# Performance work log

Measured on AMD Instinct MI355X. Metric: run time of the kernel, lower is better.

## Reference

```python
import jax, jax.numpy as jnp
import numpy as np

D = 128      # embedding_dim
E = 50000    # positive edges per metapath
S = 16       # negative samples per edge
N_A = 100000 # nodes of type A (head type of both metapaths)
N_B = 50000  # nodes of type B (tail type of metapath 1)


def setup_inputs() -> dict:
    key = jax.random.key(0)
    ks = jax.random.split(key, 10)
    emb_A = jax.random.normal(ks[0], (N_A, D), dtype=jnp.float32)
    emb_B = jax.random.normal(ks[1], (N_B, D), dtype=jnp.float32)
    # nn.init.uniform_(a=-1, b=1)
    rel_emb = jax.random.uniform(ks[2], (2, D, D), dtype=jnp.float32, minval=-1.0, maxval=1.0)
    edge_index_m0 = jax.random.randint(ks[3], (2, E), 0, N_A)  # A -> A
    edge_index_m1 = jnp.stack([
        jax.random.randint(ks[4], (E,), 0, N_A),               # heads: type A
        jax.random.randint(ks[5], (E,), 0, N_B),               # tails: type B
    ])
    neg_head_m0 = jax.random.randint(ks[6], (E, S), 0, N_A)
    neg_head_m1 = jax.random.randint(ks[7], (E, S), 0, N_A)
    neg_tail_m0 = jax.random.randint(ks[8], (E, S), 0, N_A)
    neg_tail_m1 = jax.random.randint(ks[9], (E, S), 0, N_B)
    return dict(emb_A=emb_A, emb_B=emb_B, rel_emb=rel_emb,
                edge_index_m0=edge_index_m0, edge_index_m1=edge_index_m1,
                neg_head_m0=neg_head_m0, neg_head_m1=neg_head_m1,
                neg_tail_m0=neg_tail_m0, neg_tail_m1=neg_tail_m1)


# The torch module computes score = (A K B^T).sum(dim=1); summing the [E,E]
# score matrix over dim 1 equals contracting with sum_j b_j, so we never
# materialize the [E,E] (or [E*S, E*S]) matrix -- same math, fused reduction.

def _pos_score(K, emb_h, emb_t, edge_index):
    s = emb_t[edge_index[1]].sum(0)          # [d] = sum_j b_j
    return emb_h[edge_index[0]] @ (K @ s)    # [E]


def _neg_head_score(K, emb_h, neg):
    # predict(mode='head'): emb_A = emb_h[neg.reshape(-1)],
    # idx_B = edge_index[0][arange(E)*S] == neg[:, 0],
    # side_B = (K @ emb_h[idx_B].T).repeat_interleave(S, -1); sum over columns
    # == K @ (S * sum_j emb_h[neg[j, 0]]).
    s = neg.shape[1]
    c = K @ (s * emb_h[neg[:, 0]].sum(0))    # [d]
    return emb_h[neg.reshape(-1)] @ c        # [E*S]


def _neg_tail_score(K, emb_t, neg):
    # predict(mode='tail'): emb_B = emb_t[neg.reshape(-1)],
    # idx_A = edge_index[1][arange(E)*S] == neg[:, 0],
    # side_A = (emb_t[idx_A] @ K).repeat_interleave(S, 0); row sums of
    # side_A @ emb_B^T == side_A @ sum_j emb_B[j].
    s = neg.shape[1]
    sb = emb_t[neg.reshape(-1)].sum(0)       # [d]
    base = (emb_t[neg[:, 0]] @ K) @ sb       # [E]
    return jnp.repeat(base, s)               # [E*S]


def reference(emb_A, emb_B, rel_emb, edge_index_m0, edge_index_m1,
              neg_head_m0, neg_head_m1, neg_tail_m0, neg_tail_m1):
    K0, K1 = rel_emb[0], rel_emb[1]
    pos0 = _pos_score(K0, emb_A, emb_A, edge_index_m0)   # [E]
    pos1 = _pos_score(K1, emb_A, emb_B, edge_index_m1)   # [E]
    nh0 = _neg_head_score(K0, emb_A, neg_head_m0)        # [E*S]
    nh1 = _neg_head_score(K1, emb_A, neg_head_m1)        # [E*S]
    nt0 = _neg_tail_score(K0, emb_A, neg_tail_m0)        # [E*S]
    nt1 = _neg_tail_score(K1, emb_B, neg_tail_m1)        # [E*S]
    return jnp.concatenate([pos0, pos1, nh0, nh1, nt0, nt1])
```

## Files before the change

kernel.cpp:

```cpp
#include <hip/hip_runtime.h>
#include <stdint.h>

#define D 128
#define E_EDGES 50000
#define S_NEG 16
#define N_A 100000
#define N_B 50000
#define ES (E_EDGES * S_NEG)

#define CHUNK 12500
#define B_SLABS 68
#define GA 1344
#define GB 704
#define RA 42
#define RB 22


__global__ void k_hist(const int* __restrict__ ei0, const int* __restrict__ ei1,
                       const int* __restrict__ nh0, const int* __restrict__ nh1,
                       const int* __restrict__ nt0, const int* __restrict__ nt1,
                       uint32_t* __restrict__ partA, uint32_t* __restrict__ partB) {
    __shared__ uint32_t h[CHUNK];
    const int tid = threadIdx.x;
    for (int w = tid; w < CHUNK; w += 256) h[w] = 0;
    __syncthreads();

    const int b = blockIdx.x;
    const int* src; long long base; int stride, lo; uint32_t* dst;
    if (b < 8) {
        const int c = b >> 1, hh = b & 1;
        src = ei0; base = E_EDGES + (long long)c * CHUNK; stride = 1;
        lo = hh * 50000; dst = partA + (size_t)(c * 2 + hh) * CHUNK;
    } else if (b < 16) {
        const int q = b - 8, c = q >> 1, hh = q & 1;
        src = nh0; base = (long long)c * CHUNK * S_NEG; stride = S_NEG;
        lo = hh * 50000; dst = partA + (size_t)((4 + c) * 2 + hh) * CHUNK;
    } else if (b < 24) {
        const int q = b - 16, c = q >> 1, hh = q & 1;
        src = nh1; base = (long long)c * CHUNK * S_NEG; stride = S_NEG;
        lo = hh * 50000; dst = partA + (size_t)((8 + c) * 2 + hh) * CHUNK;
    } else if (b < 152) {
        const int q = b - 24, c = q >> 1, hh = q & 1;
        src = nt0; base = (long long)c * CHUNK; stride = 1;
        lo = hh * 50000; dst = partA + (size_t)((12 + c) * 2 + hh) * CHUNK;
    } else if (b < 156) {
        const int c = b - 152;
        src = ei1; base = E_EDGES + (long long)c * CHUNK; stride = 1;
        lo = 0; dst = partB + (size_t)c * CHUNK;
    } else {
        const int c = b - 156;
        src = nt1; base = (long long)c * CHUNK; stride = 1;
        lo = 0; dst = partB + (size_t)(4 + c) * CHUNK;
    }

    for (int i = tid; i < CHUNK; i += 256) {
        const unsigned r = (unsigned)(src[base + (long long)i * stride] - lo);
        if (r < 50000u) atomicAdd(&h[r >> 2], 1u << ((r & 3u) * 8u));
    }
    __syncthreads();
    for (int w = tid; w < CHUNK; w += 256) dst[w] = h[w];
}

__global__ void k_reduceC(const uint32_t* __restrict__ partA,
                          const uint32_t* __restrict__ partB,
                          int4* __restrict__ cntAi, int2* __restrict__ cntBi) {
    const int t = blockIdx.x * 256 + threadIdx.x;
    if (t < N_A) {
        const int n = t;
        const int hh = (n >= 50000);
        const int w = (n - hh * 50000) >> 2;
        const int sh = (n & 3) * 8;
        const uint32_t* p = partA + (size_t)hh * CHUNK + w;
        unsigned s0 = 0, s1 = 0, s2 = 0, s3 = 0;
#pragma unroll
        for (int c = 0; c < 4; ++c)   s0 += (p[(size_t)(c * 2) * CHUNK] >> sh) & 255u;
#pragma unroll
        for (int c = 4; c < 8; ++c)   s1 += (p[(size_t)(c * 2) * CHUNK] >> sh) & 255u;
#pragma unroll
        for (int c = 8; c < 12; ++c)  s2 += (p[(size_t)(c * 2) * CHUNK] >> sh) & 255u;
#pragma unroll 8
        for (int c = 12; c < 76; ++c) s3 += (p[(size_t)(c * 2) * CHUNK] >> sh) & 255u;
        cntAi[n] = make_int4((int)s0, (int)s1, (int)s2, (int)s3);
    } else if (t < N_A + N_B) {
        const int n = t - N_A;
        const int w = n >> 2;
        const int sh = (n & 3) * 8;
        const uint32_t* p = partB + w;
        unsigned s0 = 0, s1 = 0;
#pragma unroll
        for (int c = 0; c < 4; ++c)   s0 += (p[(size_t)c * CHUNK] >> sh) & 255u;
#pragma unroll 8
        for (int c = 4; c < 68; ++c)  s1 += (p[(size_t)c * CHUNK] >> sh) & 255u;
        cntBi[n] = make_int2((int)s0, (int)s1);
    }
}

__global__ void k_scan1(const float* __restrict__ embA, const float* __restrict__ embB,
                        const int4* __restrict__ cntAi, const int2* __restrict__ cntBi,
                        float* __restrict__ psumA, float* __restrict__ psumB) {
    __shared__ float sds[4 * D];
    const int tid = threadIdx.x;
    const int l = tid & 31;
    const int grp = tid >> 5;

    for (int j = tid; j < 4 * D; j += 256) sds[j] = 0.f;
    __syncthreads();

    if ((int)blockIdx.x < GA) {
        float a0=0,a1=0,a2=0,a3=0, b0=0,b1=0,b2=0,b3=0;
        float c0=0,c1=0,c2=0,c3=0, d0=0,d1=0,d2=0,d3=0;
        for (int n = blockIdx.x * 8 + grp; n < N_A; n += GA * 8) {
            const int4 w = cntAi[n];
            const float4 r = *reinterpret_cast<const float4*>(embA + (size_t)n * D + 4 * l);
            float f;
            f = (float)w.x; a0 += f*r.x; a1 += f*r.y; a2 += f*r.z; a3 += f*r.w;
            f = (float)w.y; b0 += f*r.x; b1 += f*r.y; b2 += f*r.z; b3 += f*r.w;
            f = (float)w.z; c0 += f*r.x; c1 += f*r.y; c2 += f*r.z; c3 += f*r.w;
            f = (float)w.w; d0 += f*r.x; d1 += f*r.y; d2 += f*r.z; d3 += f*r.w;
        }
        atomicAdd(&sds[0*D + 4*l+0], a0); atomicAdd(&sds[0*D + 4*l+1], a1);
        atomicAdd(&sds[0*D + 4*l+2], a2); atomicAdd(&sds[0*D + 4*l+3], a3);
        atomicAdd(&sds[1*D + 4*l+0], b0); atomicAdd(&sds[1*D + 4*l+1], b1);
        atomicAdd(&sds[1*D + 4*l+2], b2); atomicAdd(&sds[1*D + 4*l+3], b3);
        atomicAdd(&sds[2*D + 4*l+0], c0); atomicAdd(&sds[2*D + 4*l+1], c1);
        atomicAdd(&sds[2*D + 4*l+2], c2); atomicAdd(&sds[2*D + 4*l+3], c3);
        atomicAdd(&sds[3*D + 4*l+0], d0); atomicAdd(&sds[3*D + 4*l+1], d1);
        atomicAdd(&sds[3*D + 4*l+2], d2); atomicAdd(&sds[3*D + 4*l+3], d3);
        __syncthreads();
        for (int j = tid; j < 4 * D; j += 256)
            psumA[(size_t)blockIdx.x * 512 + j] = sds[j];
    } else {
        const int bi = blockIdx.x - GA;
        float a0=0,a1=0,a2=0,a3=0, b0=0,b1=0,b2=0,b3=0;
        for (int n = bi * 8 + grp; n < N_B; n += GB * 8) {
            const int2 w = cntBi[n];
            const float4 r = *reinterpret_cast<const float4*>(embB + (size_t)n * D + 4 * l);
            float f;
            f = (float)w.x; a0 += f*r.x; a1 += f*r.y; a2 += f*r.z; a3 += f*r.w;
            f = (float)w.y; b0 += f*r.x; b1 += f*r.y; b2 += f*r.z; b3 += f*r.w;
        }
        atomicAdd(&sds[0*D + 4*l+0], a0); atomicAdd(&sds[0*D + 4*l+1], a1);
        atomicAdd(&sds[0*D + 4*l+2], a2); atomicAdd(&sds[0*D + 4*l+3], a3);
        atomicAdd(&sds[1*D + 4*l+0], b0); atomicAdd(&sds[1*D + 4*l+1], b1);
        atomicAdd(&sds[1*D + 4*l+2], b2); atomicAdd(&sds[1*D + 4*l+3], b3);
        __syncthreads();
        for (int j = tid; j < 2 * D; j += 256)
            psumB[(size_t)bi * 256 + j] = sds[j];
    }
}

__global__ void k_red1(const float* __restrict__ psumA, const float* __restrict__ psumB,
                       float* __restrict__ psumA2, float* __restrict__ psumB2) {
    const int b = blockIdx.x, t = threadIdx.x;
    if (b < RA) {
        const float* p = psumA + (size_t)b * 32 * 512;
        float s0 = 0.f, s1 = 0.f;
#pragma unroll 8
        for (int r = 0; r < 32; ++r) { s0 += p[r * 512 + t]; s1 += p[r * 512 + 256 + t]; }
        psumA2[(size_t)b * 512 + t] = s0;
        psumA2[(size_t)b * 512 + 256 + t] = s1;
    } else {
        const int bi = b - RA;
        const float* p = psumB + (size_t)bi * 32 * 256;
        float s = 0.f;
#pragma unroll 8
        for (int r = 0; r < 32; ++r) s += p[r * 256 + t];
        psumB2[(size_t)bi * 256 + t] = s;
    }
}

__global__ void k_cvec2(const float* __restrict__ rel,
                        const float* __restrict__ psumA2, const float* __restrict__ psumB2,
                        float* __restrict__ cvec) {
    const int j = blockIdx.x;
    const int tid = threadIdx.x;
    const int g = tid >> 7, i = tid & 127;
    __shared__ float red[256];
    __shared__ float sv[D];

    float s = 0.f;
    if (j == 1 || j == 5) {
        const int plane = (j == 1) ? 0 : 1;
        for (int b = g; b < RB; b += 2) s += psumB2[(size_t)b * 256 + plane * D + i];
    } else {
        const int plane = (j == 0) ? 0 : (j - 1);
        for (int b = g; b < RA; b += 2) s += psumA2[(size_t)b * 512 + plane * D + i];
    }
    red[tid] = s;
    __syncthreads();
    if (tid < 128) sv[i] = red[i] + red[128 + i];
    __syncthreads();

    if (tid < 128) {
        const float* Kp = rel + (size_t)(j & 1) * D * D;
        const float scale = (j == 2 || j == 3) ? (float)S_NEG : 1.0f;
        float acc = 0.f;
#pragma unroll 8
        for (int k = 0; k < D; ++k) acc += Kp[(size_t)i * D + k] * sv[k];
        cvec[j * D + i] = acc * scale;
    }
}

__global__ void k_scan2(const float* __restrict__ embA, const float* __restrict__ embB,
                        const float* __restrict__ cvec, float* __restrict__ PA,
                        float* __restrict__ PB) {
    __shared__ float sc[5 * D];
    const int tid = threadIdx.x;
    const int l = tid & 31;
    const int grp = tid >> 5;

    if ((int)blockIdx.x < GA) {
        for (int j = tid; j < 5 * D; j += 256) sc[j] = cvec[j];
        __syncthreads();
        for (int n = blockIdx.x * 8 + grp; n < N_A; n += GA * 8) {
            const float4 r = *reinterpret_cast<const float4*>(embA + (size_t)n * D + 4 * l);
            float p0 = r.x*sc[0*D+4*l] + r.y*sc[0*D+4*l+1] + r.z*sc[0*D+4*l+2] + r.w*sc[0*D+4*l+3];
            float p1 = r.x*sc[1*D+4*l] + r.y*sc[1*D+4*l+1] + r.z*sc[1*D+4*l+2] + r.w*sc[1*D+4*l+3];
            float p2 = r.x*sc[2*D+4*l] + r.y*sc[2*D+4*l+1] + r.z*sc[2*D+4*l+2] + r.w*sc[2*D+4*l+3];
            float p3 = r.x*sc[3*D+4*l] + r.y*sc[3*D+4*l+1] + r.z*sc[3*D+4*l+2] + r.w*sc[3*D+4*l+3];
            float p4 = r.x*sc[4*D+4*l] + r.y*sc[4*D+4*l+1] + r.z*sc[4*D+4*l+2] + r.w*sc[4*D+4*l+3];
#pragma unroll
            for (int m = 1; m <= 16; m <<= 1) {
                p0 += __shfl_xor(p0, m);
                p1 += __shfl_xor(p1, m);
                p2 += __shfl_xor(p2, m);
                p3 += __shfl_xor(p3, m);
                p4 += __shfl_xor(p4, m);
            }
            if (l == 0) {
                float* o = PA + (size_t)n * 5;
                o[0] = p0; o[1] = p1; o[2] = p2; o[3] = p3; o[4] = p4;
            }
        }
    } else {
        for (int j = tid; j < D; j += 256) sc[j] = cvec[5 * D + j];
        __syncthreads();
        const int bi = blockIdx.x - GA;
        for (int n = bi * 8 + grp; n < N_B; n += GB * 8) {
            const float4 r = *reinterpret_cast<const float4*>(embB + (size_t)n * D + 4 * l);
            float p = r.x*sc[4*l] + r.y*sc[4*l+1] + r.z*sc[4*l+2] + r.w*sc[4*l+3];
#pragma unroll
            for (int m = 1; m <= 16; m <<= 1) p += __shfl_xor(p, m);
            if (l == 0) PB[n] = p;
        }
    }
}

__global__ void k_scatter(const int* __restrict__ ei0, const int* __restrict__ ei1,
                          const int* __restrict__ nh0, const int* __restrict__ nh1,
                          const int* __restrict__ nt0, const int* __restrict__ nt1,
                          const float* __restrict__ PA, const float* __restrict__ PB,
                          float* __restrict__ out) {
    const int total = 2 * E_EDGES + 4 * ES;
    for (int t = blockIdx.x * blockDim.x + threadIdx.x; t < total;
         t += gridDim.x * blockDim.x) {
        float v;
        if (t < E_EDGES) {
            v = PA[(size_t)ei0[t] * 5 + 0];
        } else if (t < 2 * E_EDGES) {
            v = PA[(size_t)ei1[t - E_EDGES] * 5 + 1];
        } else if (t < 2 * E_EDGES + ES) {
            v = PA[(size_t)nh0[t - 2 * E_EDGES] * 5 + 2];
        } else if (t < 2 * E_EDGES + 2 * ES) {
            v = PA[(size_t)nh1[t - 2 * E_EDGES - ES] * 5 + 3];
        } else if (t < 2 * E_EDGES + 3 * ES) {
            const int i = t - 2 * E_EDGES - 2 * ES;
            v = PA[(size_t)nt0[(i >> 4) << 4] * 5 + 4];
        } else {
            const int i = t - 2 * E_EDGES - 3 * ES;
            v = PB[nt1[(i >> 4) << 4]];
        }
        out[t] = v;
    }
}

extern "C" void kernel_launch(void* const* d_in, const int* in_sizes, int n_in,
                              void* d_out, int out_size, void* d_ws, size_t ws_size,
                              hipStream_t stream) {
    const float* embA = (const float*)d_in[0];
    const float* embB = (const float*)d_in[1];
    const float* rel  = (const float*)d_in[2];
    const int* ei0 = (const int*)d_in[3];
    const int* ei1 = (const int*)d_in[4];
    const int* nh0 = (const int*)d_in[5];
    const int* nh1 = (const int*)d_in[6];
    const int* nt0 = (const int*)d_in[7];
    const int* nt1 = (const int*)d_in[8];
    float* out = (float*)d_out;

    uint32_t* partA = (uint32_t*)d_ws;
    uint32_t* partB = partA + (size_t)152 * CHUNK;
    int4* cntAi = (int4*)(partB + (size_t)B_SLABS * CHUNK);
    int2* cntBi = (int2*)(cntAi + N_A);
    float* psumA = (float*)(cntBi + N_B);
    float* psumB = psumA + (size_t)GA * 512;
    float* psumA2 = psumB + (size_t)GB * 256;
    float* psumB2 = psumA2 + (size_t)RA * 512;
    float* cvec  = psumB2 + (size_t)RB * 256;
    float* PA    = cvec + 6 * D;
    float* PB    = PA + (size_t)N_A * 5;

    k_hist<<<220, 256, 0, stream>>>(ei0, ei1, nh0, nh1, nt0, nt1, partA, partB);
    k_reduceC<<<(N_A + N_B + 255) / 256, 256, 0, stream>>>(partA, partB, cntAi, cntBi);
    k_scan1<<<GA + GB, 256, 0, stream>>>(embA, embB, cntAi, cntBi, psumA, psumB);
    k_red1<<<RA + RB, 256, 0, stream>>>(psumA, psumB, psumA2, psumB2);
    k_cvec2<<<6, 256, 0, stream>>>(rel, psumA2, psumB2, cvec);
    k_scan2<<<GA + GB, 256, 0, stream>>>(embA, embB, cvec, PA, PB);
    k_scatter<<<4096, 256, 0, stream>>>(ei0, ei1, nh0, nh1, nt0, nt1, PA, PB, out);
}
```

Baseline: 233.2 us.

## Restructure embedding scans into contiguous row chunks, vectorize scatter, stage K in LDS

```diff
diff --git a/kernel.cpp b/kernel.cpp
--- a/kernel.cpp
+++ b/kernel.cpp
@@ -10,10 +10,17 @@
 
 #define CHUNK 12500
 #define B_SLABS 68
-#define GA 1344
-#define GB 704
-#define RA 42
-#define RB 22
+#define GA 512
+#define GB 256
+#define RPG 25
+#define RA 16
+#define RB 8
+
+__device__ inline float dot4(float4 a, float4 b) {
+    return a.x * b.x + a.y * b.y + a.z * b.z + a.w * b.w;
+}
+#define RED32(p) { p += __shfl_xor(p, 1); p += __shfl_xor(p, 2); p += __shfl_xor(p, 4); \
+                   p += __shfl_xor(p, 8); p += __shfl_xor(p, 16); }
 
 
 __global__ void k_hist(const int* __restrict__ ei0, const int* __restrict__ ei1,
@@ -63,7 +70,7 @@
 
 __global__ void k_reduceC(const uint32_t* __restrict__ partA,
                           const uint32_t* __restrict__ partB,
-                          int4* __restrict__ cntAi, int2* __restrict__ cntBi) {
+                          float4* __restrict__ cwA, float2* __restrict__ cwB) {
     const int t = blockIdx.x * 256 + threadIdx.x;
     if (t < N_A) {
         const int n = t;
@@ -80,7 +87,7 @@
         for (int c = 8; c < 12; ++c)  s2 += (p[(size_t)(c * 2) * CHUNK] >> sh) & 255u;
 #pragma unroll 8
         for (int c = 12; c < 76; ++c) s3 += (p[(size_t)(c * 2) * CHUNK] >> sh) & 255u;
-        cntAi[n] = make_int4((int)s0, (int)s1, (int)s2, (int)s3);
+        cwA[n] = make_float4((float)s0, (float)s1, (float)s2, (float)s3);
     } else if (t < N_A + N_B) {
         const int n = t - N_A;
         const int w = n >> 2;
@@ -91,12 +98,12 @@
         for (int c = 0; c < 4; ++c)   s0 += (p[(size_t)c * CHUNK] >> sh) & 255u;
 #pragma unroll 8
         for (int c = 4; c < 68; ++c)  s1 += (p[(size_t)c * CHUNK] >> sh) & 255u;
-        cntBi[n] = make_int2((int)s0, (int)s1);
+        cwB[n] = make_float2((float)s0, (float)s1);
     }
 }
 
 __global__ void k_scan1(const float* __restrict__ embA, const float* __restrict__ embB,
-                        const int4* __restrict__ cntAi, const int2* __restrict__ cntBi,
+                        const float4* __restrict__ cwA, const float2* __restrict__ cwB,
                         float* __restrict__ psumA, float* __restrict__ psumB) {
     __shared__ float sds[4 * D];
     const int tid = threadIdx.x;
@@ -107,45 +114,85 @@
     __syncthreads();
 
     if ((int)blockIdx.x < GA) {
-        float a0=0,a1=0,a2=0,a3=0, b0=0,b1=0,b2=0,b3=0;
-        float c0=0,c1=0,c2=0,c3=0, d0=0,d1=0,d2=0,d3=0;
-        for (int n = blockIdx.x * 8 + grp; n < N_A; n += GA * 8) {
-            const int4 w = cntAi[n];
-            const float4 r = *reinterpret_cast<const float4*>(embA + (size_t)n * D + 4 * l);
-            float f;
-            f = (float)w.x; a0 += f*r.x; a1 += f*r.y; a2 += f*r.z; a3 += f*r.w;
-            f = (float)w.y; b0 += f*r.x; b1 += f*r.y; b2 += f*r.z; b3 += f*r.w;
-            f = (float)w.z; c0 += f*r.x; c1 += f*r.y; c2 += f*r.z; c3 += f*r.w;
-            f = (float)w.w; d0 += f*r.x; d1 += f*r.y; d2 += f*r.z; d3 += f*r.w;
-        }
-        atomicAdd(&sds[0*D + 4*l+0], a0); atomicAdd(&sds[0*D + 4*l+1], a1);
-        atomicAdd(&sds[0*D + 4*l+2], a2); atomicAdd(&sds[0*D + 4*l+3], a3);
-        atomicAdd(&sds[1*D + 4*l+0], b0); atomicAdd(&sds[1*D + 4*l+1], b1);
-        atomicAdd(&sds[1*D + 4*l+2], b2); atomicAdd(&sds[1*D + 4*l+3], b3);
-        atomicAdd(&sds[2*D + 4*l+0], c0); atomicAdd(&sds[2*D + 4*l+1], c1);
-        atomicAdd(&sds[2*D + 4*l+2], c2); atomicAdd(&sds[2*D + 4*l+3], c3);
-        atomicAdd(&sds[3*D + 4*l+0], d0); atomicAdd(&sds[3*D + 4*l+1], d1);
-        atomicAdd(&sds[3*D + 4*l+2], d2); atomicAdd(&sds[3*D + 4*l+3], d3);
+        const int gid = blockIdx.x * 8 + grp;
+        int r = gid * RPG;
+        const int end = min(r + RPG, N_A);
+        float acc[16];
+#pragma unroll
+        for (int k = 0; k < 16; ++k) acc[k] = 0.f;
+        const float* base = embA + 4 * l;
+        for (; r + 4 <= end; r += 4) {
+            float4 w[4], x[4];
+#pragma unroll
+            for (int u = 0; u < 4; ++u) w[u] = cwA[r + u];
+#pragma unroll
+            for (int u = 0; u < 4; ++u)
+                x[u] = *reinterpret_cast<const float4*>(base + (size_t)(r + u) * D);
+#pragma unroll
+            for (int u = 0; u < 4; ++u) {
+                acc[0]  += w[u].x * x[u].x; acc[1]  += w[u].x * x[u].y;
+                acc[2]  += w[u].x * x[u].z; acc[3]  += w[u].x * x[u].w;
+                acc[4]  += w[u].y * x[u].x; acc[5]  += w[u].y * x[u].y;
+                acc[6]  += w[u].y * x[u].z; acc[7]  += w[u].y * x[u].w;
+                acc[8]  += w[u].z * x[u].x; acc[9]  += w[u].z * x[u].y;
+                acc[10] += w[u].z * x[u].z; acc[11] += w[u].z * x[u].w;
+                acc[12] += w[u].w * x[u].x; acc[13] += w[u].w * x[u].y;
+                acc[14] += w[u].w * x[u].z; acc[15] += w[u].w * x[u].w;
+            }
+        }
+        for (; r < end; ++r) {
+            const float4 w0 = cwA[r];
+            const float4 x0 = *reinterpret_cast<const float4*>(base + (size_t)r * D);
+            acc[0]  += w0.x * x0.x; acc[1]  += w0.x * x0.y; acc[2]  += w0.x * x0.z; acc[3]  += w0.x * x0.w;
+            acc[4]  += w0.y * x0.x; acc[5]  += w0.y * x0.y; acc[6]  += w0.y * x0.z; acc[7]  += w0.y * x0.w;
+            acc[8]  += w0.z * x0.x; acc[9]  += w0.z * x0.y; acc[10] += w0.z * x0.z; acc[11] += w0.z * x0.w;
+            acc[12] += w0.w * x0.x; acc[13] += w0.w * x0.y; acc[14] += w0.w * x0.z; acc[15] += w0.w * x0.w;
+        }
+#pragma unroll
+        for (int p = 0; p < 4; ++p)
+#pragma unroll
+            for (int k = 0; k < 4; ++k)
+                atomicAdd(&sds[p * D + 4 * l + k], acc[p * 4 + k]);
         __syncthreads();
         for (int j = tid; j < 4 * D; j += 256)
             psumA[(size_t)blockIdx.x * 512 + j] = sds[j];
     } else {
-        const int bi = blockIdx.x - GA;
-        float a0=0,a1=0,a2=0,a3=0, b0=0,b1=0,b2=0,b3=0;
-        for (int n = bi * 8 + grp; n < N_B; n += GB * 8) {
-            const int2 w = cntBi[n];
-            const float4 r = *reinterpret_cast<const float4*>(embB + (size_t)n * D + 4 * l);
-            float f;
-            f = (float)w.x; a0 += f*r.x; a1 += f*r.y; a2 += f*r.z; a3 += f*r.w;
-            f = (float)w.y; b0 += f*r.x; b1 += f*r.y; b2 += f*r.z; b3 += f*r.w;
-        }
-        atomicAdd(&sds[0*D + 4*l+0], a0); atomicAdd(&sds[0*D + 4*l+1], a1);
-        atomicAdd(&sds[0*D + 4*l+2], a2); atomicAdd(&sds[0*D + 4*l+3], a3);
-        atomicAdd(&sds[1*D + 4*l+0], b0); atomicAdd(&sds[1*D + 4*l+1], b1);
-        atomicAdd(&sds[1*D + 4*l+2], b2); atomicAdd(&sds[1*D + 4*l+3], b3);
+        const int gid = (blockIdx.x - GA) * 8 + grp;
+        int r = gid * RPG;
+        const int end = min(r + RPG, N_B);
+        float acc[8];
+#pragma unroll
+        for (int k = 0; k < 8; ++k) acc[k] = 0.f;
+        const float* base = embB + 4 * l;
+        for (; r + 4 <= end; r += 4) {
+            float2 w[4]; float4 x[4];
+#pragma unroll
+            for (int u = 0; u < 4; ++u) w[u] = cwB[r + u];
+#pragma unroll
+            for (int u = 0; u < 4; ++u)
+                x[u] = *reinterpret_cast<const float4*>(base + (size_t)(r + u) * D);
+#pragma unroll
+            for (int u = 0; u < 4; ++u) {
+                acc[0] += w[u].x * x[u].x; acc[1] += w[u].x * x[u].y;
+                acc[2] += w[u].x * x[u].z; acc[3] += w[u].x * x[u].w;
+                acc[4] += w[u].y * x[u].x; acc[5] += w[u].y * x[u].y;
+                acc[6] += w[u].y * x[u].z; acc[7] += w[u].y * x[u].w;
+            }
+        }
+        for (; r < end; ++r) {
+            const float2 w0 = cwB[r];
+            const float4 x0 = *reinterpret_cast<const float4*>(base + (size_t)r * D);
+            acc[0] += w0.x * x0.x; acc[1] += w0.x * x0.y; acc[2] += w0.x * x0.z; acc[3] += w0.x * x0.w;
+            acc[4] += w0.y * x0.x; acc[5] += w0.y * x0.y; acc[6] += w0.y * x0.z; acc[7] += w0.y * x0.w;
+        }
+#pragma unroll
+        for (int p = 0; p < 2; ++p)
+#pragma unroll
+            for (int k = 0; k < 4; ++k)
+                atomicAdd(&sds[p * D + 4 * l + k], acc[p * 4 + k]);
         __syncthreads();
         for (int j = tid; j < 2 * D; j += 256)
-            psumB[(size_t)bi * 256 + j] = sds[j];
+            psumB[(size_t)(blockIdx.x - GA) * 256 + j] = sds[j];
     }
 }
 
@@ -174,10 +221,19 @@
                         float* __restrict__ cvec) {
     const int j = blockIdx.x;
     const int tid = threadIdx.x;
-    const int g = tid >> 7, i = tid & 127;
+    __shared__ float Kds[D * 129];
     __shared__ float red[256];
     __shared__ float sv[D];
-
+    const float* Kp = rel + (size_t)(j & 1) * D * D;
+
+    for (int e = tid; e < D * D / 4; e += 256) {
+        const int row = e >> 5, col = (e & 31) * 4;
+        const float4 v = *reinterpret_cast<const float4*>(Kp + (size_t)row * D + col);
+        float* dst = Kds + row * 129 + col;
+        dst[0] = v.x; dst[1] = v.y; dst[2] = v.z; dst[3] = v.w;
+    }
+
+    const int g = tid >> 7, i = tid & 127;
     float s = 0.f;
     if (j == 1 || j == 5) {
         const int plane = (j == 1) ? 0 : 1;
@@ -192,11 +248,12 @@
     __syncthreads();
 
     if (tid < 128) {
-        const float* Kp = rel + (size_t)(j & 1) * D * D;
         const float scale = (j == 2 || j == 3) ? (float)S_NEG : 1.0f;
         float acc = 0.f;
-#pragma unroll 8
-        for (int k = 0; k < D; ++k) acc += Kp[(size_t)i * D + k] * sv[k];
+#pragma unroll
+        for (int k = 0; k < D; k += 4)
+            acc += Kds[i * 129 + k] * sv[k] + Kds[i * 129 + k + 1] * sv[k + 1]
+                 + Kds[i * 129 + k + 2] * sv[k + 2] + Kds[i * 129 + k + 3] * sv[k + 3];
         cvec[j * D + i] = acc * scale;
     }
 }
@@ -212,36 +269,69 @@
     if ((int)blockIdx.x < GA) {
         for (int j = tid; j < 5 * D; j += 256) sc[j] = cvec[j];
         __syncthreads();
-        for (int n = blockIdx.x * 8 + grp; n < N_A; n += GA * 8) {
-            const float4 r = *reinterpret_cast<const float4*>(embA + (size_t)n * D + 4 * l);
-            float p0 = r.x*sc[0*D+4*l] + r.y*sc[0*D+4*l+1] + r.z*sc[0*D+4*l+2] + r.w*sc[0*D+4*l+3];
-            float p1 = r.x*sc[1*D+4*l] + r.y*sc[1*D+4*l+1] + r.z*sc[1*D+4*l+2] + r.w*sc[1*D+4*l+3];
-            float p2 = r.x*sc[2*D+4*l] + r.y*sc[2*D+4*l+1] + r.z*sc[2*D+4*l+2] + r.w*sc[2*D+4*l+3];
-            float p3 = r.x*sc[3*D+4*l] + r.y*sc[3*D+4*l+1] + r.z*sc[3*D+4*l+2] + r.w*sc[3*D+4*l+3];
-            float p4 = r.x*sc[4*D+4*l] + r.y*sc[4*D+4*l+1] + r.z*sc[4*D+4*l+2] + r.w*sc[4*D+4*l+3];
-#pragma unroll
-            for (int m = 1; m <= 16; m <<= 1) {
-                p0 += __shfl_xor(p0, m);
-                p1 += __shfl_xor(p1, m);
-                p2 += __shfl_xor(p2, m);
-                p3 += __shfl_xor(p3, m);
-                p4 += __shfl_xor(p4, m);
+        float4 cf[5];
+#pragma unroll
+        for (int p = 0; p < 5; ++p)
+            cf[p] = *reinterpret_cast<const float4*>(sc + p * D + 4 * l);
+        const int gid = blockIdx.x * 8 + grp;
+        int r = gid * RPG;
+        const int end = min(r + RPG, N_A);
+        const float* base = embA + 4 * l;
+        for (; r + 4 <= end; r += 4) {
+            float4 x[4];
+#pragma unroll
+            for (int u = 0; u < 4; ++u)
+                x[u] = *reinterpret_cast<const float4*>(base + (size_t)(r + u) * D);
+            float p_[4][5];
+#pragma unroll
+            for (int u = 0; u < 4; ++u)
+#pragma unroll
+                for (int p = 0; p < 5; ++p) p_[u][p] = dot4(x[u], cf[p]);
+#pragma unroll
+            for (int u = 0; u < 4; ++u)
+#pragma unroll
+                for (int p = 0; p < 5; ++p) RED32(p_[u][p]);
+            if (l < 4) {
+                float* o = PA + (size_t)(r + l) * 5;
+#pragma unroll
+                for (int p = 0; p < 5; ++p)
+                    o[p] = (l == 1) ? p_[1][p] : (l == 2) ? p_[2][p] : (l == 3) ? p_[3][p] : p_[0][p];
             }
+        }
+        for (; r < end; ++r) {
+            const float4 x0 = *reinterpret_cast<const float4*>(base + (size_t)r * D);
+            float q[5];
+#pragma unroll
+            for (int p = 0; p < 5; ++p) { q[p] = dot4(x0, cf[p]); RED32(q[p]); }
             if (l == 0) {
-                float* o = PA + (size_t)n * 5;
-                o[0] = p0; o[1] = p1; o[2] = p2; o[3] = p3; o[4] = p4;
+                float* o = PA + (size_t)r * 5;
+#pragma unroll
+                for (int p = 0; p < 5; ++p) o[p] = q[p];
             }
         }
     } else {
         for (int j = tid; j < D; j += 256) sc[j] = cvec[5 * D + j];
         __syncthreads();
-        const int bi = blockIdx.x - GA;
-        for (int n = bi * 8 + grp; n < N_B; n += GB * 8) {
-            const float4 r = *reinterpret_cast<const float4*>(embB + (size_t)n * D + 4 * l);
-            float p = r.x*sc[4*l] + r.y*sc[4*l+1] + r.z*sc[4*l+2] + r.w*sc[4*l+3];
-#pragma unroll
-            for (int m = 1; m <= 16; m <<= 1) p += __shfl_xor(p, m);
-            if (l == 0) PB[n] = p;
+        const float4 cf = *reinterpret_cast<const float4*>(sc + 4 * l);
+        const int gid = (blockIdx.x - GA) * 8 + grp;
+        int r = gid * RPG;
+        const int end = min(r + RPG, N_B);
+        const float* base = embB + 4 * l;
+        for (; r + 4 <= end; r += 4) {
+            float4 x[4];
+#pragma unroll
+            for (int u = 0; u < 4; ++u)
+                x[u] = *reinterpret_cast<const float4*>(base + (size_t)(r + u) * D);
+            float p_[4];
+#pragma unroll
+            for (int u = 0; u < 4; ++u) { p_[u] = dot4(x[u], cf); RED32(p_[u]); }
+            if (l < 4)
+                PB[r + l] = (l == 1) ? p_[1] : (l == 2) ? p_[2] : (l == 3) ? p_[3] : p_[0];
+        }
+        for (; r < end; ++r) {
+            const float4 x0 = *reinterpret_cast<const float4*>(base + (size_t)r * D);
+            float q = dot4(x0, cf); RED32(q);
+            if (l == 0) PB[r] = q;
         }
     }
 }
@@ -251,26 +341,37 @@
                           const int* __restrict__ nt0, const int* __restrict__ nt1,
                           const float* __restrict__ PA, const float* __restrict__ PB,
                           float* __restrict__ out) {
-    const int total = 2 * E_EDGES + 4 * ES;
-    for (int t = blockIdx.x * blockDim.x + threadIdx.x; t < total;
+    const int total4 = (2 * E_EDGES + 4 * ES) / 4;
+    for (int t = blockIdx.x * blockDim.x + threadIdx.x; t < total4;
          t += gridDim.x * blockDim.x) {
-        float v;
-        if (t < E_EDGES) {
-            v = PA[(size_t)ei0[t] * 5 + 0];
-        } else if (t < 2 * E_EDGES) {
-            v = PA[(size_t)ei1[t - E_EDGES] * 5 + 1];
-        } else if (t < 2 * E_EDGES + ES) {
-            v = PA[(size_t)nh0[t - 2 * E_EDGES] * 5 + 2];
-        } else if (t < 2 * E_EDGES + 2 * ES) {
-            v = PA[(size_t)nh1[t - 2 * E_EDGES - ES] * 5 + 3];
-        } else if (t < 2 * E_EDGES + 3 * ES) {
-            const int i = t - 2 * E_EDGES - 2 * ES;
-            v = PA[(size_t)nt0[(i >> 4) << 4] * 5 + 4];
+        const int e = t * 4;
+        float4 v;
+        if (e < E_EDGES) {
+            const int4 i4 = *reinterpret_cast<const int4*>(ei0 + e);
+            v = make_float4(PA[(size_t)i4.x * 5], PA[(size_t)i4.y * 5],
+                            PA[(size_t)i4.z * 5], PA[(size_t)i4.w * 5]);
+        } else if (e < 2 * E_EDGES) {
+            const int4 i4 = *reinterpret_cast<const int4*>(ei1 + (e - E_EDGES));
+            v = make_float4(PA[(size_t)i4.x * 5 + 1], PA[(size_t)i4.y * 5 + 1],
+                            PA[(size_t)i4.z * 5 + 1], PA[(size_t)i4.w * 5 + 1]);
+        } else if (e < 2 * E_EDGES + ES) {
+            const int4 i4 = *reinterpret_cast<const int4*>(nh0 + (e - 2 * E_EDGES));
+            v = make_float4(PA[(size_t)i4.x * 5 + 2], PA[(size_t)i4.y * 5 + 2],
+                            PA[(size_t)i4.z * 5 + 2], PA[(size_t)i4.w * 5 + 2]);
+        } else if (e < 2 * E_EDGES + 2 * ES) {
+            const int4 i4 = *reinterpret_cast<const int4*>(nh1 + (e - 2 * E_EDGES - ES));
+            v = make_float4(PA[(size_t)i4.x * 5 + 3], PA[(size_t)i4.y * 5 + 3],
+                            PA[(size_t)i4.z * 5 + 3], PA[(size_t)i4.w * 5 + 3]);
+        } else if (e < 2 * E_EDGES + 3 * ES) {
+            const int i = e - 2 * E_EDGES - 2 * ES;
+            const float s = PA[(size_t)nt0[(i >> 4) << 4] * 5 + 4];
+            v = make_float4(s, s, s, s);
         } else {
-            const int i = t - 2 * E_EDGES - 3 * ES;
-            v = PB[nt1[(i >> 4) << 4]];
-        }
-        out[t] = v;
+            const int i = e - 2 * E_EDGES - 3 * ES;
+            const float s = PB[nt1[(i >> 4) << 4]];
+            v = make_float4(s, s, s, s);
+        }
+        *reinterpret_cast<float4*>(out + e) = v;
     }
 }
 
@@ -290,9 +391,9 @@
 
     uint32_t* partA = (uint32_t*)d_ws;
     uint32_t* partB = partA + (size_t)152 * CHUNK;
-    int4* cntAi = (int4*)(partB + (size_t)B_SLABS * CHUNK);
-    int2* cntBi = (int2*)(cntAi + N_A);
-    float* psumA = (float*)(cntBi + N_B);
+    float4* cwA = (float4*)(partB + (size_t)B_SLABS * CHUNK);
+    float2* cwB = (float2*)(cwA + N_A);
+    float* psumA = (float*)(cwB + N_B);
     float* psumB = psumA + (size_t)GA * 512;
     float* psumA2 = psumB + (size_t)GB * 256;
     float* psumB2 = psumA2 + (size_t)RA * 512;
@@ -301,10 +402,10 @@
     float* PB    = PA + (size_t)N_A * 5;
 
     k_hist<<<220, 256, 0, stream>>>(ei0, ei1, nh0, nh1, nt0, nt1, partA, partB);
-    k_reduceC<<<(N_A + N_B + 255) / 256, 256, 0, stream>>>(partA, partB, cntAi, cntBi);
-    k_scan1<<<GA + GB, 256, 0, stream>>>(embA, embB, cntAi, cntBi, psumA, psumB);
+    k_reduceC<<<(N_A + N_B + 255) / 256, 256, 0, stream>>>(partA, partB, cwA, cwB);
+    k_scan1<<<GA + GB, 256, 0, stream>>>(embA, embB, cwA, cwB, psumA, psumB);
     k_red1<<<RA + RB, 256, 0, stream>>>(psumA, psumB, psumA2, psumB2);
     k_cvec2<<<6, 256, 0, stream>>>(rel, psumA2, psumB2, cvec);
     k_scan2<<<GA + GB, 256, 0, stream>>>(embA, embB, cvec, PA, PB);
-    k_scatter<<<4096, 256, 0, stream>>>(ei0, ei1, nh0, nh1, nt0, nt1, PA, PB, out);
-}
+    k_scatter<<<2048, 256, 0, stream>>>(ei0, ei1, nh0, nh1, nt0, nt1, PA, PB, out);
+}
```

New measurement: 214.7 us. 1.09x faster.
